# Performance work log

Hardware: AMD Instinct MI355X
Metric: run time of the kernel (lower is better)

Reference implementation:

```python
import jax, jax.numpy as jnp
import numpy as np

B, DIM, RANK, H, W = 16, 64, 32, 128, 128
E, K, BINS, FREQ_DIM, KS = 4, 2, 8, 64, 7
NOISE_STD = 1.0 / E


def dwconv(x, w, b, pad):
    # depthwise conv, NCHW, weight [C,1,kh,kw]
    y = jax.lax.conv_general_dilated(x, w, (1, 1), [(pad, pad), (pad, pad)],
        dimension_numbers=('NCHW', 'OIHW', 'NCHW'), feature_group_count=x.shape[1])
    return y + b[None, :, None, None]


def avgpool3(x):
    # AvgPool2d(3, stride=1, padding=1), count_include_pad=True -> sum/9
    s = jax.lax.reduce_window(x, 0.0, jax.lax.add, (1, 1, 3, 3), (1, 1, 1, 1),
        [(0, 0), (0, 0), (1, 1), (1, 1)])
    return s / 9.0


def freq_filter(x, gain, decay, cmax):
    # HighFreqGlobal / LowFreqGlobal: rfft2 -> scale magnitude by radial filter -> irfft2
    Bh, C, Hh, Wh = x.shape
    xf = jnp.fft.rfft2(x, norm='ortho')
    mag, ph = jnp.abs(xf), jnp.angle(xf)
    fy = jnp.fft.fftfreq(Hh).astype(x.dtype)[:, None]
    fx = jnp.fft.rfftfreq(Wh).astype(x.dtype)[None, :]
    fg = jnp.sqrt(fy ** 2 + fx ** 2)
    filt = jnp.clip((1.0 - jnp.exp(-gain * fg)) * jnp.exp(-decay * fg), 0.0, cmax)
    return jnp.fft.irfft2((mag * filt) * jnp.exp(1j * ph), s=(Hh, Wh), norm='ortho')


def freq_energy(x):
    # RoutingFunction.get_frequency_energy: radial energy histogram over BINS bins
    Bh, C, Hh, Wh = x.shape
    mag = jnp.abs(jnp.fft.fft2(x, norm='forward'))
    gy = jnp.arange(-Hh // 2, Hh // 2, dtype=jnp.float32)[:, None]
    gx = jnp.arange(-Wh // 2, Wh // 2, dtype=jnp.float32)[None, :]
    dist = jnp.sqrt(gy ** 2 + gx ** 2)
    edges = jnp.linspace(0.0, dist.max(), BINS + 1)
    masks = ((dist[None] >= edges[:-1, None, None]) & (dist[None] < edges[1:, None, None])).astype(mag.dtype)
    return jnp.einsum('bchw,khw->bk', mag, masks) / C  # sum over HW then mean over C


def setup_inputs():
    key = jax.random.key(0)
    ks = jax.random.split(key, 16)
    p = lambda k, shp, s=0.02: jax.random.normal(k, shp, jnp.float32) * s
    return {
        'x': jax.random.normal(ks[0], (B, DIM, H, W), jnp.float32),
        'noise': jax.random.normal(ks[1], (B, E), jnp.float32),
        'gate_w': p(ks[2], (E, DIM)),
        'fg_w1': p(ks[3], (FREQ_DIM, BINS)),
        'fg_b1': jnp.zeros((FREQ_DIM,), jnp.float32),
        'fg_w2': p(ks[4], (E, FREQ_DIM)),
        'proj0': p(ks[5], (E, RANK, DIM)),
        'proj1': p(ks[6], (E, RANK, DIM)),
        'proj2': p(ks[7], (E, DIM, RANK)),
        'hg_gain': jnp.float32(2.0),
        'hg_decay': jnp.float32(0.5),
        'hf_w1': p(ks[8], (RANK, 1, 3, 3), 0.1),
        'hf_b1': jnp.zeros((RANK,), jnp.float32),
        'hf_w2': p(ks[9], (RANK, 1, 3, 3), 0.1),
        'hf_b2': jnp.zeros((RANK,), jnp.float32),
        'lg_gain': jnp.float32(1.0),
        'lg_decay': jnp.float32(1.0),
        'lf_w': p(ks[10], (RANK, 1, KS, KS), 0.1),
        'lf_b': jnp.zeros((RANK,), jnp.float32),
    }


def reference(x, noise, gate_w, fg_w1, fg_b1, fg_w2, proj0, proj1, proj2,
              hg_gain, hg_decay, hf_w1, hf_b1, hf_w2, hf_b2,
              lg_gain, lg_decay, lf_w, lf_b):
    Bh = x.shape[0]
    # routing: image gate (GAP + linear) + frequency gate (MLP on radial energy)
    img_logits = jnp.mean(x, axis=(2, 3)) @ gate_w.T
    femb = freq_energy(x)
    hidden = jax.nn.relu(femb @ fg_w1.T + fg_b1)
    logits = img_logits + hidden @ fg_w2.T
    scores = jax.nn.softmax(logits + noise * NOISE_STD, axis=-1)
    vals, idx = jax.lax.top_k(scores, K)
    gates = jnp.zeros_like(scores).at[jnp.arange(Bh)[:, None], idx].set(vals)

    def expert(e, body):
        # ModExpert.process: low-rank proj -> body * silu(gate proj of shared=x) -> up proj + shortcut
        h = jnp.einsum('bchw,rc->brhw', x, proj0[e])
        g = jax.nn.silu(jnp.einsum('bchw,rc->brhw', x, proj1[e]))
        h = body(h) * g
        return jnp.einsum('brhw,cr->bchw', h, proj2[e]) + x

    gelu = lambda z: jax.nn.gelu(z, approximate=False)
    bodies = [
        lambda z: freq_filter(z, hg_gain, hg_decay, 3.0),                          # HighFreqGlobal
        lambda z: dwconv(gelu(dwconv(z, hf_w1, hf_b1, 1)), hf_w2, hf_b2, 1),       # HighFreqLocal
        lambda z: freq_filter(z, lg_gain, lg_decay, 1.0),                          # LowFreqGlobal
        lambda z: avgpool3(gelu(dwconv(z, lf_w, lf_b, KS // 2))),                  # LowFreqLocal
    ]
    # dispatch/combine expressed densely: gates are exactly zero for non-selected experts,
    # so weighted sum == SparseDispatcher.combine
    out = jnp.zeros_like(x)
    for e, body in enumerate(bodies):
        out = out + gates[:, e][:, None, None, None] * expert(e, body)
    return out
```

## Files before the change

### kernel.cpp

```cpp
#include <hip/hip_runtime.h>
#include <math.h>


namespace {

struct cpx { float x, y; };
struct TwB {
  cpx t0;
  cpx ws[6];
  float sg[6];
};

using bf16x8 = __attribute__((ext_vector_type(8))) short;
using f32x4  = __attribute__((ext_vector_type(4))) float;

__device__ __forceinline__ short f2bf(float f){
  unsigned u = __float_as_uint(f);
  u += 0x7FFF + ((u >> 16) & 1);
  return (short)(u >> 16);
}

__device__ __forceinline__ cpx cmul(cpx a, cpx b){ return {a.x*b.x - a.y*b.y, a.x*b.y + a.y*b.x}; }

__device__ __forceinline__ cpx tw(int k, float invN){
  float s, c;
  sincosf(-6.283185307179586f * (float)k * invN, &s, &c);
  return {c, s};
}

__device__ __forceinline__ void init_twb(TwB &T, int lane){
  T.t0 = tw(lane, 1.0f/128.0f);
  int m = 32;
  #pragma unroll
  for (int s = 0; s < 6; s++){
    bool up = (lane & m) != 0;
    cpx w = tw(lane & (m-1), 1.0f/(float)(2*m));
    T.ws[s] = up ? w : cpx{1.0f, 0.0f};
    T.sg[s] = up ? -1.0f : 1.0f;
    m >>= 1;
  }
}

__device__ __forceinline__ int br6(int l){ return (int)(__brev((unsigned)l) >> 26); }
__device__ __forceinline__ int pos7(int j){ return ((j & 1) << 6) | (j >> 1); }

__device__ __forceinline__ void fft128(cpx &a, cpx &b, int lane, const TwB &T){
  cpx u{a.x + b.x, a.y + b.y};
  cpx v{a.x - b.x, a.y - b.y};
  v = cmul(v, T.t0);
  a = u; b = v;
  int m = 32;
  #pragma unroll
  for (int s = 0; s < 6; s++){
    float pax = __shfl_xor(a.x, m);
    float pay = __shfl_xor(a.y, m);
    float pbx = __shfl_xor(b.x, m);
    float pby = __shfl_xor(b.y, m);
    float sg = T.sg[s];
    cpx w = T.ws[s];
    cpx ta{fmaf(sg, a.x, pax), fmaf(sg, a.y, pay)};
    cpx tb{fmaf(sg, b.x, pbx), fmaf(sg, b.y, pby)};
    a = cmul(ta, w);
    b = cmul(tb, w);
    m >>= 1;
  }
}

__device__ __forceinline__ float gelu_exact(float v){
  return 0.5f * v * (1.0f + erff(v * 0.70710678118654752f));
}

__device__ __forceinline__ float silu(float v){
  return v / (1.0f + expf(-v));
}


__global__ __launch_bounds__(512) void k_fft2fwd(const float* __restrict__ x, float2* __restrict__ X,
                                                 float* __restrict__ part_w, float* __restrict__ xmean){
  __shared__ float2 z[8192];
  int bc = blockIdx.x; int t = threadIdx.x;
  int lane = t & 63, wv = t >> 6;
  TwB T; init_twb(T, lane);
  const float* img = x + (size_t)bc * 16384;
  int rb = br6(lane);

  #pragma unroll 4
  for (int k = 0; k < 8; k++){
    int p = wv*8 + k;
    int h0 = 2*p, h1 = 2*p + 1;
    cpx a{img[h0*128 + lane],      img[h1*128 + lane]};
    cpx b{img[h0*128 + lane + 64], img[h1*128 + lane + 64]};
    fft128(a, b, lane, T);
    int ia = (p << 7) | (rb ^ p);
    z[ia]      = make_float2(a.x, a.y);
    z[ia | 64] = make_float2(b.x, b.y);
  }
  __syncthreads();

  float rax[8], ray[8], rbx[8], rby[8];
  #pragma unroll
  for (int k = 0; k < 8; k++){
    int jj = wv*8 + k;
    int p  = lane >> 1, s = lane & 1;
    int p2 = 32 + p;
    cpx a, b;
    if (jj == 0){
      float2 z0  = z[(p << 7)  | (0  ^ p)];
      float2 z64 = z[(p << 7)  | (32 ^ p)];
      float2 w0  = z[(p2 << 7) | (0  ^ p2)];
      float2 w64 = z[(p2 << 7) | (32 ^ p2)];
      a = { s ? z0.y : z0.x, s ? z64.y : z64.x };
      b = { s ? w0.y : w0.x, s ? w64.y : w64.x };
    } else {
      int jm = 128 - jj;
      int pj = pos7(jj), pm = pos7(jm);
      float2 z1 = z[(p << 7) | (pj ^ p)],  z2 = z[(p << 7) | (pm ^ p)];
      if (s == 0) a = { 0.5f*(z1.x + z2.x), 0.5f*(z1.y - z2.y) };
      else        a = { 0.5f*(z1.y + z2.y), 0.5f*(z2.x - z1.x) };
      float2 w1 = z[(p2 << 7) | (pj ^ p2)], w2 = z[(p2 << 7) | (pm ^ p2)];
      if (s == 0) b = { 0.5f*(w1.x + w2.x), 0.5f*(w1.y - w2.y) };
      else        b = { 0.5f*(w1.y + w2.y), 0.5f*(w2.x - w1.x) };
    }
    fft128(a, b, lane, T);
    rax[k] = a.x; ray[k] = a.y; rbx[k] = b.x; rby[k] = b.y;
  }
  __syncthreads();
  #pragma unroll
  for (int k = 0; k < 8; k++){
    int jj = wv*8 + k;
    int ia = (jj << 7) | (rb ^ jj);
    z[ia]      = make_float2(rax[k], ray[k]);
    z[ia | 64] = make_float2(rbx[k], rby[k]);
  }
  __syncthreads();

  if (t == 0) xmean[bc] = z[0].x * (1.0f/16384.0f);

  float edges[9];
  float step = sqrtf(8192.0f) * 0.125f;
  #pragma unroll
  for (int k = 0; k <= 8; k++) edges[k] = step * (float)k;
  float acc[8] = {0,0,0,0,0,0,0,0};
  for (int idx = t; idx < 64*128; idx += 512){
    int j = idx >> 7, i = idx & 127;
    if (j == 0){
      float2 c0 = z[pos7(i)];
      int in_ = (128 - i) & 127;
      float2 d0v = z[pos7(in_)];
      float x0r = 0.5f*(c0.x + d0v.x), x0i = 0.5f*(c0.y - d0v.y);
      float x6r = 0.5f*(c0.y + d0v.y), x6i = 0.5f*(d0v.x - c0.x);
      float m0 = sqrtf(x0r*x0r + x0i*x0i) * (1.0f/16384.0f);
      float m6 = sqrtf(x6r*x6r + x6i*x6i) * (1.0f/16384.0f);
      float dyv = (float)(i - 64);
      float d0 = sqrtf(dyv*dyv + 4096.0f);
      float d6 = fabsf(dyv);
      #pragma unroll
      for (int k = 0; k < 8; k++){
        if (d0 >= edges[k] && d0 < edges[k+1]) acc[k] += m0;
        if (d6 >= edges[k] && d6 < edges[k+1]) acc[k] += m6;
      }
    } else {
      float2 zv = z[(j << 7) | (pos7(i) ^ j)];
      float mag = sqrtf(zv.x*zv.x + zv.y*zv.y) * (2.0f/16384.0f);
      float dy = (float)(i - 64), dx = (float)(j - 64);
      float d = sqrtf(dy*dy + dx*dx);
      #pragma unroll
      for (int k = 0; k < 8; k++)
        if (d >= edges[k] && d < edges[k+1]) acc[k] += mag;
    }
  }
  #pragma unroll
  for (int k = 0; k < 8; k++){
    float v = acc[k];
    for (int off = 32; off > 0; off >>= 1) v += __shfl_xor(v, off);
    if (lane == 0) part_w[(bc*8 + wv)*8 + k] = v;
  }

  float2* Xo = X + (size_t)bc * (65*128);
  for (int idx = t; idx < 65*128; idx += 512){
    int j = idx >> 7, i = idx & 127;
    float2 v;
    if (j == 0){
      float2 c0 = z[pos7(i)];
      int in_ = (128 - i) & 127;
      float2 d0v = z[pos7(in_)];
      v = make_float2(0.5f*(c0.x + d0v.x), 0.5f*(c0.y - d0v.y));
    } else if (j == 64){
      float2 c0 = z[pos7(i)];
      int in_ = (128 - i) & 127;
      float2 d0v = z[pos7(in_)];
      v = make_float2(0.5f*(c0.y + d0v.y), 0.5f*(d0v.x - c0.x));
    } else {
      v = z[(j << 7) | (pos7(i) ^ j)];
    }
    Xo[idx] = v;
  }
}

__global__ __launch_bounds__(128) void k_routing(const float* __restrict__ xmean, const float* __restrict__ part_w,
    const float* __restrict__ noise, const float* __restrict__ gate_w,
    const float* __restrict__ fg_w1, const float* __restrict__ fg_b1, const float* __restrict__ fg_w2,
    int* __restrict__ slot_e, int* __restrict__ slot_of, float* __restrict__ slot_g){
  __shared__ float femb[16][8];
  __shared__ float hid[16][64];
  __shared__ float lgt[16][4];
  int t = threadIdx.x;
  {
    int b = t >> 3, k = t & 7;
    float s = 0.f;
    for (int c = 0; c < 64; c++)
      for (int w = 0; w < 8; w++)
        s += part_w[((b*64 + c)*8 + w)*8 + k];
    femb[b][k] = s * (1.0f/64.0f);
  }
  __syncthreads();
  for (int idx = t; idx < 16*64; idx += 128){
    int b = idx >> 6, f = idx & 63;
    float s = fg_b1[f];
    for (int k = 0; k < 8; k++) s += femb[b][k] * fg_w1[f*8 + k];
    hid[b][f] = fmaxf(s, 0.f);
  }
  __syncthreads();
  if (t < 64){
    int b = t >> 2, e = t & 3;
    float s = 0.f;
    for (int c = 0; c < 64; c++) s += xmean[b*64 + c] * gate_w[e*64 + c];
    for (int f = 0; f < 64; f++) s += hid[b][f] * fg_w2[e*64 + f];
    lgt[b][e] = s + noise[b*4 + e] * 0.25f;
  }
  __syncthreads();
  if (t < 16){
    int b = t;
    float m = fmaxf(fmaxf(lgt[b][0], lgt[b][1]), fmaxf(lgt[b][2], lgt[b][3]));
    float p[4]; float sum = 0.f;
    for (int e = 0; e < 4; e++){ p[e] = expf(lgt[b][e] - m); sum += p[e]; }
    for (int e = 0; e < 4; e++) p[e] /= sum;
    int i1 = 0;
    for (int e = 1; e < 4; e++) if (p[e] > p[i1]) i1 = e;
    int i2 = -1;
    for (int e = 0; e < 4; e++){ if (e == i1) continue; if (i2 < 0 || p[e] > p[i2]) i2 = e; }
    slot_e[b*2 + 0] = i1;
    slot_e[b*2 + 1] = i2;
    slot_g[b*2 + 0] = p[i1];
    slot_g[b*2 + 1] = p[i2];
    for (int e = 0; e < 4; e++) slot_of[b*4 + e] = (e == i1) ? 0 : ((e == i2) ? 1 : -1);
  }
}

__global__ __launch_bounds__(256) void k_transW(const float* __restrict__ proj0, float* __restrict__ p0t){
  int t = threadIdx.x;
  for (int idx = t; idx < 2048; idx += 256){
    int r = idx >> 6, c = idx & 63;
    p0t[0*2048 + c*32 + r] = proj0[0*2048 + idx];
    p0t[1*2048 + c*32 + r] = proj0[2*2048 + idx];
  }
}

__global__ __launch_bounds__(256) void k_projfreq(const float2* __restrict__ X, const float* __restrict__ p0t,
    float2* __restrict__ Y, const int* __restrict__ slot_e,
    const float* __restrict__ hg_gain, const float* __restrict__ hg_decay,
    const float* __restrict__ lg_gain, const float* __restrict__ lg_decay){
  int b = blockIdx.z;
  int e0 = __builtin_amdgcn_readfirstlane(slot_e[b*2 + 0]);
  int e1 = __builtin_amdgcn_readfirstlane(slot_e[b*2 + 1]);
  bool f0 = (e0 == 0) || (e0 == 2);
  bool f1 = (e1 == 0) || (e1 == 2);
  if (!f0 && !f1) return;
  int j = blockIdx.y;
  int i0 = blockIdx.x * 64;
  int t = threadIdx.x;
  int lane = t & 63;
  int w = __builtin_amdgcn_readfirstlane(t >> 6);
  __shared__ float2 sx[64][64];
  for (int idx = t; idx < 4096; idx += 256){
    int c = idx >> 6, ii = idx & 63;
    sx[c][ii] = X[(((size_t)(b*64 + c))*65 + j)*128 + i0 + ii];
  }
  __syncthreads();
  int i = i0 + lane;
  const float* W0 = p0t + ((f0 ? (e0 >> 1) : (e1 >> 1)) * 2048) + w*8;
  const float* W1 = p0t + ((f1 ? (e1 >> 1) : (e0 >> 1)) * 2048) + w*8;
  float a0x[8] = {0,0,0,0,0,0,0,0}, a0y[8] = {0,0,0,0,0,0,0,0};
  float a1x[8] = {0,0,0,0,0,0,0,0}, a1y[8] = {0,0,0,0,0,0,0,0};
  for (int c = 0; c < 64; c++){
    float2 xv = sx[c][lane];
    const float* wc0 = W0 + c*32;
    const float* wc1 = W1 + c*32;
    #pragma unroll
    for (int k = 0; k < 8; k++){
      float w0v = wc0[k];
      a0x[k] += w0v * xv.x; a0y[k] += w0v * xv.y;
      float w1v = wc1[k];
      a1x[k] += w1v * xv.x; a1y[k] += w1v * xv.y;
    }
  }
  float fy = (float)(i < 64 ? i : i - 128) * (1.0f/128.0f);
  float fx = (float)j * (1.0f/128.0f);
  float fg = sqrtf(fy*fy + fx*fx);
  if (f0){
    float gain, decay, cmax;
    if (e0 == 0){ gain = *hg_gain; decay = *hg_decay; cmax = 3.0f; }
    else        { gain = *lg_gain; decay = *lg_decay; cmax = 1.0f; }
    float filt = (1.0f - expf(-gain*fg)) * expf(-decay*fg);
    filt = fminf(fmaxf(filt, 0.0f), cmax) * (1.0f/16384.0f);
    int bs = b*2 + 0;
    #pragma unroll
    for (int k = 0; k < 8; k++){
      int r = w*8 + k;
      Y[((size_t)(bs*32 + r))*8320 + j*128 + i] = make_float2(a0x[k]*filt, a0y[k]*filt);
    }
  }
  if (f1){
    float gain, decay, cmax;
    if (e1 == 0){ gain = *hg_gain; decay = *hg_decay; cmax = 3.0f; }
    else        { gain = *lg_gain; decay = *lg_decay; cmax = 1.0f; }
    float filt = (1.0f - expf(-gain*fg)) * expf(-decay*fg);
    filt = fminf(fmaxf(filt, 0.0f), cmax) * (1.0f/16384.0f);
    int bs = b*2 + 1;
    #pragma unroll
    for (int k = 0; k < 8; k++){
      int r = w*8 + k;
      Y[((size_t)(bs*32 + r))*8320 + j*128 + i] = make_float2(a1x[k]*filt, a1y[k]*filt);
    }
  }
}

__global__ __launch_bounds__(512) void k_ifft2(float2* __restrict__ Y, const int* __restrict__ slot_e){
  int blk = blockIdx.x;
  int bs = blk >> 5, r = blk & 31;
  int es = slot_e[bs];
  if (es == 1 || es == 3) return;
  __shared__ float2 z[8192];
  int t = threadIdx.x; int lane = t & 63, wv = t >> 6;
  TwB T; init_twb(T, lane);
  int rb = br6(lane);
  float2* Yb = Y + (size_t)(bs*32 + r) * 8320;

  for (int idx = t; idx < 8192; idx += 512){
    int j = idx >> 7, i = idx & 127;
    if (j == 0){
      float2 y0 = Yb[i];
      float2 y6 = Yb[8192 + i];
      z[pos7(i)] = make_float2(y0.x - y6.y, y0.y + y6.x);
    } else {
      z[(j << 7) | (pos7(i) ^ j)] = Yb[idx];
    }
  }
  __syncthreads();

  #pragma unroll
  for (int k = 0; k < 8; k++){
    int jj = wv*8 + k;
    float2 z0 = z[(jj << 7) | (pos7(lane) ^ jj)];
    float2 z1 = z[(jj << 7) | ((pos7(lane) + 32) ^ jj)];
    cpx a{z0.x, -z0.y}, b{z1.x, -z1.y};
    fft128(a, b, lane, T);
    int ia = (jj << 7) | (rb ^ jj);
    z[ia]      = make_float2(a.x, -a.y);
    z[ia | 64] = make_float2(b.x, -b.y);
  }
  __syncthreads();

  float* body = (float*)Yb;
  #pragma unroll 2
  for (int k = 0; k < 8; k++){
    int p = wv*8 + k;
    int h = 2*p, h1 = 2*p + 1;
    int ph = pos7(h), ph1 = pos7(h1);
    cpx a, b;
    if (lane == 0){
      float2 c0 = z[ph], c1 = z[ph1];
      a = { c0.x, c1.x };
      b = { c0.y, c1.y };
    } else {
      float2 yh = z[(lane << 7) | (ph ^ lane)];
      float2 y1 = z[(lane << 7) | (ph1 ^ lane)];
      a = { yh.x - y1.y, yh.y + y1.x };
      int lm = 64 - lane;
      float2 zh  = z[(lm << 7) | (ph ^ lm)];
      float2 z1_ = z[(lm << 7) | (ph1 ^ lm)];
      b = { zh.x + z1_.y, z1_.x - zh.y };
    }
    a.y = -a.y; b.y = -b.y;
    fft128(a, b, lane, T);
    int n0 = 2*rb;
    body[h*128 + n0]      = a.x;
    body[h1*128 + n0]     = -a.y;
    body[h*128 + n0 + 1]  = b.x;
    body[h1*128 + n0 + 1] = -b.y;
  }
}

__global__ __launch_bounds__(256) void k_projA(const float* __restrict__ x, const float* __restrict__ proj0,
    const int* __restrict__ slot_e, float* __restrict__ A){
  int b = blockIdx.y;
  int e0 = __builtin_amdgcn_readfirstlane(slot_e[b*2 + 0]);
  int e1 = __builtin_amdgcn_readfirstlane(slot_e[b*2 + 1]);
  bool c0 = (e0 == 1) || (e0 == 3);
  bool c1 = (e1 == 1) || (e1 == 3);
  if (!c0 && !c1) return;
  __shared__ unsigned short xs[128][72];
  int px0 = blockIdx.x * 128;
  int t = threadIdx.x;
  int w = t >> 6, lane = t & 63;
  int h = lane & 15, g = lane >> 4;
  const float* xb = x + (size_t)b*64*16384;

  for (int idx = t; idx < 2048; idx += 256){
    int c = idx >> 5, pq = idx & 31;
    float4 v = *(const float4*)&xb[(size_t)c*16384 + px0 + pq*4];
    xs[pq*4 + 0][c] = (unsigned short)f2bf(v.x);
    xs[pq*4 + 1][c] = (unsigned short)f2bf(v.y);
    xs[pq*4 + 2][c] = (unsigned short)f2bf(v.z);
    xs[pq*4 + 3][c] = (unsigned short)f2bf(v.w);
  }

  bf16x8 af[2][2][2];
  #pragma unroll
  for (int s = 0; s < 2; s++){
    bool cv = (s == 0) ? c0 : c1;
    if (!cv) continue;
    int e = (s == 0) ? e0 : e1;
    const float* P0 = proj0 + e*2048;
    #pragma unroll
    for (int mr = 0; mr < 2; mr++)
      #pragma unroll
      for (int k0 = 0; k0 < 2; k0++){
        const float* p = P0 + (mr*16 + h)*64 + k0*32 + g*8;
        bf16x8 v;
        #pragma unroll
        for (int j = 0; j < 8; j++) v[j] = f2bf(p[j]);
        af[s][mr][k0] = v;
      }
  }
  __syncthreads();

  int pxw = w*32;
  #pragma unroll
  for (int nt = 0; nt < 2; nt++){
    int pxl = pxw + nt*16;
    int px  = px0 + pxl;
    bf16x8 bx[2];
    #pragma unroll
    for (int k0 = 0; k0 < 2; k0++)
      bx[k0] = *(bf16x8*)&xs[pxl + h][k0*32 + g*8];
    #pragma unroll
    for (int s = 0; s < 2; s++){
      bool cv = (s == 0) ? c0 : c1;
      if (!cv) continue;
      float* Ab = A + (size_t)((b*2 + s)*32)*16384;
      #pragma unroll
      for (int mr = 0; mr < 2; mr++){
        f32x4 acc = {0.f, 0.f, 0.f, 0.f};
        acc = __builtin_amdgcn_mfma_f32_16x16x32_bf16(af[s][mr][0], bx[0], acc, 0, 0, 0);
        acc = __builtin_amdgcn_mfma_f32_16x16x32_bf16(af[s][mr][1], bx[1], acc, 0, 0, 0);
        #pragma unroll
        for (int reg = 0; reg < 4; reg++){
          int r = mr*16 + g*4 + reg;
          Ab[(size_t)r*16384 + px + h] = acc[reg];
        }
      }
    }
  }
}

__global__ __launch_bounds__(256) void k_conv3(const float* __restrict__ A, float* __restrict__ bodyY,
    const float* __restrict__ w1g, const float* __restrict__ b1g,
    const float* __restrict__ w2g, const float* __restrict__ b2g,
    const int* __restrict__ slot_of){
  int by = blockIdx.y; int b = by >> 5, r = by & 31;
  int slot = slot_of[b*4 + 1];
  if (slot < 0) return;
  int bs = b*2 + slot;
  int h0 = blockIdx.x * 16;
  int t = threadIdx.x;
  __shared__ float sin_[20*130];
  __shared__ float st[18*130];
  for (int i = t; i < 20*130; i += 256) sin_[i] = 0.f;
  for (int i = t; i < 18*130; i += 256) st[i] = 0.f;
  float w1[9], w2[9];
  #pragma unroll
  for (int k = 0; k < 9; k++){ w1[k] = w1g[r*9 + k]; w2[k] = w2g[r*9 + k]; }
  float b1 = b1g[r], b2 = b2g[r];
  __syncthreads();
  const float* ip = A + (size_t)(bs*32 + r)*16384;
  for (int idx = t; idx < 20*128; idx += 256){
    int li = idx >> 7, ww = idx & 127;
    int ih = h0 - 2 + li;
    if (ih >= 0 && ih < 128) sin_[li*130 + 1 + ww] = ip[ih*128 + ww];
  }
  __syncthreads();
  for (int idx = t; idx < 18*128; idx += 256){
    int li = idx >> 7, ww = idx & 127;
    int hs = h0 - 1 + li;
    if (hs >= 0 && hs < 128){
      float acc = b1;
      #pragma unroll
      for (int kh = 0; kh < 3; kh++)
        #pragma unroll
        for (int kw = 0; kw < 3; kw++)
          acc += w1[kh*3 + kw] * sin_[(li + kh)*130 + ww + kw];
      st[li*130 + 1 + ww] = gelu_exact(acc);
    }
  }
  __syncthreads();
  float* op = bodyY + (size_t)(bs*32 + r)*16640;
  for (int idx = t; idx < 16*128; idx += 256){
    int li = idx >> 7, ww = idx & 127;
    int ho = h0 + li;
    float acc = b2;
    #pragma unroll
    for (int kh = 0; kh < 3; kh++)
      #pragma unroll
      for (int kw = 0; kw < 3; kw++)
        acc += w2[kh*3 + kw] * st[(li + kh)*130 + ww + kw];
    op[ho*128 + ww] = acc;
  }
}

__global__ __launch_bounds__(256) void k_conv7(const float* __restrict__ A, float* __restrict__ bodyY,
    const float* __restrict__ wg, const float* __restrict__ bg,
    const int* __restrict__ slot_of){
  int by = blockIdx.y; int b = by >> 5, r = by & 31;
  int slot = slot_of[b*4 + 3];
  if (slot < 0) return;
  int bs = b*2 + slot;
  int h0 = blockIdx.x * 16;
  int t = threadIdx.x;
  __shared__ float sin_[24*134];
  __shared__ float st[18*134];
  __shared__ float wsh[49];
  for (int i = t; i < 24*134; i += 256) sin_[i] = 0.f;
  for (int i = t; i < 18*134; i += 256) st[i] = 0.f;
  if (t < 49) wsh[t] = wg[r*49 + t];
  float bias = bg[r];
  __syncthreads();
  const float* ip = A + (size_t)(bs*32 + r)*16384;
  for (int idx = t; idx < 24*128; idx += 256){
    int li = idx >> 7, ww = idx & 127;
    int ih = h0 - 4 + li;
    if (ih >= 0 && ih < 128) sin_[li*134 + 3 + ww] = ip[ih*128 + ww];
  }
  __syncthreads();
  for (int idx = t; idx < 18*128; idx += 256){
    int li = idx >> 7, ww = idx & 127;
    int hs = h0 - 1 + li;
    if (hs >= 0 && hs < 128){
      float acc = bias;
      #pragma unroll
      for (int kh = 0; kh < 7; kh++)
        #pragma unroll
        for (int kw = 0; kw < 7; kw++)
          acc += wsh[kh*7 + kw] * sin_[(li + kh)*134 + ww + kw];
      st[li*134 + 1 + ww] = gelu_exact(acc);
    }
  }
  __syncthreads();
  float* op = bodyY + (size_t)(bs*32 + r)*16640;
  for (int idx = t; idx < 16*128; idx += 256){
    int li = idx >> 7, ww = idx & 127;
    int ho = h0 + li;
    float acc = 0.f;
    #pragma unroll
    for (int kh = 0; kh < 3; kh++)
      #pragma unroll
      for (int kw = 0; kw < 3; kw++)
        acc += st[(li + kh)*134 + ww + kw];
    op[ho*128 + ww] = acc * (1.0f/9.0f);
  }
}

__global__ __launch_bounds__(256) void k_combine(const float* __restrict__ x, const float* __restrict__ bodyY,
    const float* __restrict__ proj1, const float* __restrict__ proj2,
    const int* __restrict__ slot_e, const float* __restrict__ slot_g,
    float* __restrict__ out){
  __shared__ unsigned short xs[128][72];
  __shared__ unsigned short bs2[2][128][36];
  __shared__ unsigned short sblk[4][2][16][40];
  int b = blockIdx.y;
  int px0 = blockIdx.x * 128;
  int t = threadIdx.x;
  int w = t >> 6, lane = t & 63;
  int h = lane & 15, g = lane >> 4;
  int ea = __builtin_amdgcn_readfirstlane(slot_e[b*2 + 0]);
  int eb = __builtin_amdgcn_readfirstlane(slot_e[b*2 + 1]);
  float ga = slot_g[b*2 + 0], gb = slot_g[b*2 + 1];
  float gs = ga + gb;

  const float* xb = x + (size_t)b*64*16384;
  float* ob = out + (size_t)b*64*16384;
  const float* Bd0 = bodyY + (size_t)(b*2 + 0)*32*16640;
  const float* Bd1 = bodyY + (size_t)(b*2 + 1)*32*16640;

  for (int idx = t; idx < 2048; idx += 256){
    int c = idx >> 5, pq = idx & 31;
    float4 v = *(const float4*)&xb[(size_t)c*16384 + px0 + pq*4];
    xs[pq*4 + 0][c] = (unsigned short)f2bf(v.x);
    xs[pq*4 + 1][c] = (unsigned short)f2bf(v.y);
    xs[pq*4 + 2][c] = (unsigned short)f2bf(v.z);
    xs[pq*4 + 3][c] = (unsigned short)f2bf(v.w);
  }
  for (int idx = t; idx < 2048; idx += 256){
    int s = idx >> 10, r = (idx >> 5) & 31, pq = idx & 31;
    const float* Bod = (s == 0) ? Bd0 : Bd1;
    float4 v = *(const float4*)&Bod[(size_t)r*16640 + px0 + pq*4];
    bs2[s][pq*4 + 0][r] = (unsigned short)f2bf(v.x);
    bs2[s][pq*4 + 1][r] = (unsigned short)f2bf(v.y);
    bs2[s][pq*4 + 2][r] = (unsigned short)f2bf(v.z);
    bs2[s][pq*4 + 3][r] = (unsigned short)f2bf(v.w);
  }

  bf16x8 a1[2][2][2];
  #pragma unroll
  for (int s = 0; s < 2; s++){
    const float* P1 = proj1 + (s == 0 ? ea : eb)*2048;
    #pragma unroll
    for (int mr = 0; mr < 2; mr++)
      #pragma unroll
      for (int k0 = 0; k0 < 2; k0++){
        const float* p = P1 + (mr*16 + h)*64 + k0*32 + g*8;
        bf16x8 v;
        #pragma unroll
        for (int j = 0; j < 8; j++) v[j] = f2bf(p[j]);
        a1[s][mr][k0] = v;
      }
  }
  bf16x8 a2[2][4];
  #pragma unroll
  for (int s = 0; s < 2; s++){
    const float* P2 = proj2 + (s == 0 ? ea : eb)*2048;
    #pragma unroll
    for (int mc = 0; mc < 4; mc++){
      const float* p = P2 + (mc*16 + h)*32 + g*8;
      bf16x8 v;
      #pragma unroll
      for (int j = 0; j < 8; j++) v[j] = f2bf(p[j]);
      a2[s][mc] = v;
    }
  }
  __syncthreads();

  int pxw = w*32;
  #pragma unroll
  for (int nt = 0; nt < 2; nt++){
    int pxl = pxw + nt*16;
    int px  = px0 + pxl;
    bf16x8 bx[2];
    #pragma unroll
    for (int k0 = 0; k0 < 2; k0++)
      bx[k0] = *(bf16x8*)&xs[pxl + h][k0*32 + g*8];
    f32x4 acc1[2][2];
    #pragma unroll
    for (int s = 0; s < 2; s++)
      #pragma unroll
      for (int mr = 0; mr < 2; mr++){
        f32x4 acc = {0.f, 0.f, 0.f, 0.f};
        acc = __builtin_amdgcn_mfma_f32_16x16x32_bf16(a1[s][mr][0], bx[0], acc, 0, 0, 0);
        acc = __builtin_amdgcn_mfma_f32_16x16x32_bf16(a1[s][mr][1], bx[1], acc, 0, 0, 0);
        acc1[s][mr] = acc;
      }
    #pragma unroll
    for (int s = 0; s < 2; s++){
      float gw = (s == 0) ? ga : gb;
      #pragma unroll
      for (int mr = 0; mr < 2; mr++){
        int r0 = mr*16 + g*4;
        unsigned short b4[4];
        *(uint2*)b4 = *(uint2*)&bs2[s][pxl + h][r0];
        unsigned pk0, pk1;
        {
          float bv0 = __uint_as_float(((unsigned)b4[0]) << 16);
          float bv1 = __uint_as_float(((unsigned)b4[1]) << 16);
          float bv2 = __uint_as_float(((unsigned)b4[2]) << 16);
          float bv3 = __uint_as_float(((unsigned)b4[3]) << 16);
          float s0 = gw * bv0 * silu(acc1[s][mr][0]);
          float s1 = gw * bv1 * silu(acc1[s][mr][1]);
          float s2 = gw * bv2 * silu(acc1[s][mr][2]);
          float s3 = gw * bv3 * silu(acc1[s][mr][3]);
          pk0 = (unsigned)(unsigned short)f2bf(s0) | ((unsigned)(unsigned short)f2bf(s1) << 16);
          pk1 = (unsigned)(unsigned short)f2bf(s2) | ((unsigned)(unsigned short)f2bf(s3) << 16);
        }
        uint2 pv; pv.x = pk0; pv.y = pk1;
        *(uint2*)&sblk[w][s][h][r0] = pv;
      }
    }
    bf16x8 sb0 = *(bf16x8*)&sblk[w][0][h][g*8];
    bf16x8 sb1 = *(bf16x8*)&sblk[w][1][h][g*8];
    f32x4 acc2[4];
    #pragma unroll
    for (int mc = 0; mc < 4; mc++){
      f32x4 acc = {0.f, 0.f, 0.f, 0.f};
      acc = __builtin_amdgcn_mfma_f32_16x16x32_bf16(a2[0][mc], sb0, acc, 0, 0, 0);
      acc = __builtin_amdgcn_mfma_f32_16x16x32_bf16(a2[1][mc], sb1, acc, 0, 0, 0);
      acc2[mc] = acc;
    }
    #pragma unroll
    for (int mc = 0; mc < 4; mc++)
      #pragma unroll
      for (int reg = 0; reg < 4; reg++){
        int c = mc*16 + g*4 + reg;
        size_t o = (size_t)c*16384 + px + h;
        ob[o] = gs * xb[o] + acc2[mc][reg];
      }
  }
}

}

extern "C" void kernel_launch(void* const* d_in, const int* in_sizes, int n_in,
                              void* d_out, int out_size, void* d_ws, size_t ws_size,
                              hipStream_t stream) {
  (void)in_sizes; (void)n_in; (void)out_size; (void)ws_size;
  const float* x        = (const float*)d_in[0];
  const float* noise    = (const float*)d_in[1];
  const float* gate_w   = (const float*)d_in[2];
  const float* fg_w1    = (const float*)d_in[3];
  const float* fg_b1    = (const float*)d_in[4];
  const float* fg_w2    = (const float*)d_in[5];
  const float* proj0    = (const float*)d_in[6];
  const float* proj1    = (const float*)d_in[7];
  const float* proj2    = (const float*)d_in[8];
  const float* hg_gain  = (const float*)d_in[9];
  const float* hg_decay = (const float*)d_in[10];
  const float* hf_w1    = (const float*)d_in[11];
  const float* hf_b1    = (const float*)d_in[12];
  const float* hf_w2    = (const float*)d_in[13];
  const float* hf_b2    = (const float*)d_in[14];
  const float* lg_gain  = (const float*)d_in[15];
  const float* lg_decay = (const float*)d_in[16];
  const float* lf_w     = (const float*)d_in[17];
  const float* lf_b     = (const float*)d_in[18];
  float* out = (float*)d_out;

  float* ws = (float*)d_ws;
  float2* X  = (float2*)ws;
  float*  A  = ws;
  float*  Yf = ws + 17039360;
  float2* Y2 = (float2*)Yf;
  float*  tail   = ws + 34078720;
  float*  xmean  = tail;
  float*  part_w = xmean + 1024;
  float*  p0t    = part_w + 65536;
  float*  slot_g = p0t + 4096;
  int*    slot_e = (int*)(slot_g + 32);
  int*    slot_of = slot_e + 32;

  k_transW<<<1, 256, 0, stream>>>(proj0, p0t);
  k_fft2fwd<<<1024, 512, 0, stream>>>(x, X, part_w, xmean);
  k_routing<<<1, 128, 0, stream>>>(xmean, part_w, noise, gate_w, fg_w1, fg_b1, fg_w2,
                                   slot_e, slot_of, slot_g);

  k_projfreq<<<dim3(2,65,16), 256, 0, stream>>>(X, p0t, Y2, slot_e,
                                                hg_gain, hg_decay, lg_gain, lg_decay);

  k_projA<<<dim3(128,16), 256, 0, stream>>>(x, proj0, slot_e, A);

  k_ifft2<<<1024, 512, 0, stream>>>(Y2, slot_e);

  k_conv3<<<dim3(8,512), 256, 0, stream>>>(A, Yf, hf_w1, hf_b1, hf_w2, hf_b2, slot_of);
  k_conv7<<<dim3(8,512), 256, 0, stream>>>(A, Yf, lf_w, lf_b, slot_of);

  k_combine<<<dim3(128,16), 256, 0, stream>>>(x, Yf, proj1, proj2, slot_e, slot_g, out);
}
```

Before: 304.6 us.

## Precompute FFT twiddles into a table and stage combine output for float4 stores

Twiddle factors are now computed once by the transpose kernel into a 128-entry global table, and the FFT kernels read from that table instead of calling sincosf per lane per stage. The combine kernel now stages its MFMA results in a shared-memory buffer that aliases the earlier tiles, then writes the output with coalesced float4 loads and stores that fuse in the shortcut term. This replaces the old scattered per-element global writes. It adds a __syncthreads and a larger shared footprint, which may lower occupancy.

```diff
diff --git a/kernel.cpp b/kernel.cpp
--- a/kernel.cpp
+++ b/kernel.cpp
@@ -22,20 +22,15 @@
 
 __device__ __forceinline__ cpx cmul(cpx a, cpx b){ return {a.x*b.x - a.y*b.y, a.x*b.y + a.y*b.x}; }
 
-__device__ __forceinline__ cpx tw(int k, float invN){
-  float s, c;
-  sincosf(-6.283185307179586f * (float)k * invN, &s, &c);
-  return {c, s};
-}
-
-__device__ __forceinline__ void init_twb(TwB &T, int lane){
-  T.t0 = tw(lane, 1.0f/128.0f);
+__device__ __forceinline__ void init_twb(TwB &T, int lane, const float2* __restrict__ tw128){
+  float2 v0 = tw128[lane];
+  T.t0 = {v0.x, v0.y};
   int m = 32;
   #pragma unroll
   for (int s = 0; s < 6; s++){
     bool up = (lane & m) != 0;
-    cpx w = tw(lane & (m-1), 1.0f/(float)(2*m));
-    T.ws[s] = up ? w : cpx{1.0f, 0.0f};
+    float2 wv = tw128[(lane & (m-1)) * (64/m)];
+    T.ws[s] = up ? cpx{wv.x, wv.y} : cpx{1.0f, 0.0f};
     T.sg[s] = up ? -1.0f : 1.0f;
     m >>= 1;
   }
@@ -75,12 +70,28 @@
 }
 
 
+__global__ __launch_bounds__(256) void k_transW(const float* __restrict__ proj0, float* __restrict__ p0t,
+                                                float2* __restrict__ tw128){
+  int t = threadIdx.x;
+  if (t < 128){
+    float s, c;
+    sincosf(-6.283185307179586f * (float)t * (1.0f/128.0f), &s, &c);
+    tw128[t] = make_float2(c, s);
+  }
+  for (int idx = t; idx < 2048; idx += 256){
+    int r = idx >> 6, c = idx & 63;
+    p0t[0*2048 + c*32 + r] = proj0[0*2048 + idx];
+    p0t[1*2048 + c*32 + r] = proj0[2*2048 + idx];
+  }
+}
+
 __global__ __launch_bounds__(512) void k_fft2fwd(const float* __restrict__ x, float2* __restrict__ X,
-                                                 float* __restrict__ part_w, float* __restrict__ xmean){
+                                                 float* __restrict__ part_w, float* __restrict__ xmean,
+                                                 const float2* __restrict__ tw128){
   __shared__ float2 z[8192];
   int bc = blockIdx.x; int t = threadIdx.x;
   int lane = t & 63, wv = t >> 6;
-  TwB T; init_twb(T, lane);
+  TwB T; init_twb(T, lane, tw128);
   const float* img = x + (size_t)bc * 16384;
   int rb = br6(lane);
 
@@ -247,15 +258,6 @@
   }
 }
 
-__global__ __launch_bounds__(256) void k_transW(const float* __restrict__ proj0, float* __restrict__ p0t){
-  int t = threadIdx.x;
-  for (int idx = t; idx < 2048; idx += 256){
-    int r = idx >> 6, c = idx & 63;
-    p0t[0*2048 + c*32 + r] = proj0[0*2048 + idx];
-    p0t[1*2048 + c*32 + r] = proj0[2*2048 + idx];
-  }
-}
-
 __global__ __launch_bounds__(256) void k_projfreq(const float2* __restrict__ X, const float* __restrict__ p0t,
     float2* __restrict__ Y, const int* __restrict__ slot_e,
     const float* __restrict__ hg_gain, const float* __restrict__ hg_decay,
@@ -325,14 +327,15 @@
   }
 }
 
-__global__ __launch_bounds__(512) void k_ifft2(float2* __restrict__ Y, const int* __restrict__ slot_e){
+__global__ __launch_bounds__(512) void k_ifft2(float2* __restrict__ Y, const int* __restrict__ slot_e,
+                                               const float2* __restrict__ tw128){
   int blk = blockIdx.x;
   int bs = blk >> 5, r = blk & 31;
   int es = slot_e[bs];
   if (es == 1 || es == 3) return;
   __shared__ float2 z[8192];
   int t = threadIdx.x; int lane = t & 63, wv = t >> 6;
-  TwB T; init_twb(T, lane);
+  TwB T; init_twb(T, lane, tw128);
   int rb = br6(lane);
   float2* Yb = Y + (size_t)(bs*32 + r) * 8320;
 
@@ -574,9 +577,12 @@
     const float* __restrict__ proj1, const float* __restrict__ proj2,
     const int* __restrict__ slot_e, const float* __restrict__ slot_g,
     float* __restrict__ out){
-  __shared__ unsigned short xs[128][72];
-  __shared__ unsigned short bs2[2][128][36];
-  __shared__ unsigned short sblk[4][2][16][40];
+  __shared__ __align__(16) unsigned char smem[57344];
+  unsigned short (*xs)[72]            = (unsigned short(*)[72])(smem);
+  unsigned short (*bs2)[128][36]      = (unsigned short(*)[128][36])(smem + 18432);
+  unsigned short (*sblk)[4][2][16][40] = (unsigned short(*)[4][2][16][40])(smem + 36864);
+  float* obuf = (float*)smem;
+
   int b = blockIdx.y;
   int px0 = blockIdx.x * 128;
   int t = threadIdx.x;
@@ -644,7 +650,6 @@
   #pragma unroll
   for (int nt = 0; nt < 2; nt++){
     int pxl = pxw + nt*16;
-    int px  = px0 + pxl;
     bf16x8 bx[2];
     #pragma unroll
     for (int k0 = 0; k0 < 2; k0++)
@@ -681,27 +686,38 @@
           pk1 = (unsigned)(unsigned short)f2bf(s2) | ((unsigned)(unsigned short)f2bf(s3) << 16);
         }
         uint2 pv; pv.x = pk0; pv.y = pk1;
-        *(uint2*)&sblk[w][s][h][r0] = pv;
+        *(uint2*)&sblk[nt][w][s][h][r0] = pv;
       }
     }
-    bf16x8 sb0 = *(bf16x8*)&sblk[w][0][h][g*8];
-    bf16x8 sb1 = *(bf16x8*)&sblk[w][1][h][g*8];
-    f32x4 acc2[4];
+  }
+  __syncthreads();
+
+  #pragma unroll
+  for (int nt = 0; nt < 2; nt++){
+    bf16x8 sb0 = *(bf16x8*)&sblk[nt][w][0][h][g*8];
+    bf16x8 sb1 = *(bf16x8*)&sblk[nt][w][1][h][g*8];
     #pragma unroll
     for (int mc = 0; mc < 4; mc++){
       f32x4 acc = {0.f, 0.f, 0.f, 0.f};
       acc = __builtin_amdgcn_mfma_f32_16x16x32_bf16(a2[0][mc], sb0, acc, 0, 0, 0);
       acc = __builtin_amdgcn_mfma_f32_16x16x32_bf16(a2[1][mc], sb1, acc, 0, 0, 0);
-      acc2[mc] = acc;
-    }
-    #pragma unroll
-    for (int mc = 0; mc < 4; mc++)
       #pragma unroll
       for (int reg = 0; reg < 4; reg++){
         int c = mc*16 + g*4 + reg;
-        size_t o = (size_t)c*16384 + px + h;
-        ob[o] = gs * xb[o] + acc2[mc][reg];
+        obuf[(w*64 + c)*36 + nt*16 + h] = acc[reg];
       }
+    }
+  }
+  int fq = lane & 7, cr = lane >> 3;
+  const float* xw = xb + px0 + w*32;
+  float* ow = ob + px0 + w*32;
+  #pragma unroll
+  for (int i = 0; i < 8; i++){
+    int c = i*8 + cr;
+    float4 v = *(float4*)&obuf[(w*64 + c)*36 + fq*4];
+    float4 xv4 = *(const float4*)&xw[(size_t)c*16384 + fq*4];
+    *(float4*)&ow[(size_t)c*16384 + fq*4] =
+      make_float4(gs*xv4.x + v.x, gs*xv4.y + v.y, gs*xv4.z + v.z, gs*xv4.w + v.w);
   }
 }
 
@@ -741,12 +757,14 @@
   float*  xmean  = tail;
   float*  part_w = xmean + 1024;
   float*  p0t    = part_w + 65536;
-  float*  slot_g = p0t + 4096;
+  float*  tw128f = p0t + 4096;
+  float2* tw128  = (float2*)tw128f;
+  float*  slot_g = tw128f + 256;
   int*    slot_e = (int*)(slot_g + 32);
   int*    slot_of = slot_e + 32;
 
-  k_transW<<<1, 256, 0, stream>>>(proj0, p0t);
-  k_fft2fwd<<<1024, 512, 0, stream>>>(x, X, part_w, xmean);
+  k_transW<<<1, 256, 0, stream>>>(proj0, p0t, tw128);
+  k_fft2fwd<<<1024, 512, 0, stream>>>(x, X, part_w, xmean, tw128);
   k_routing<<<1, 128, 0, stream>>>(xmean, part_w, noise, gate_w, fg_w1, fg_b1, fg_w2,
                                    slot_e, slot_of, slot_g);
 
@@ -755,7 +773,7 @@
 
   k_projA<<<dim3(128,16), 256, 0, stream>>>(x, proj0, slot_e, A);
 
-  k_ifft2<<<1024, 512, 0, stream>>>(Y2, slot_e);
+  k_ifft2<<<1024, 512, 0, stream>>>(Y2, slot_e, tw128);
 
   k_conv3<<<dim3(8,512), 256, 0, stream>>>(A, Yf, hf_w1, hf_b1, hf_w2, hf_b2, slot_of);
   k_conv7<<<dim3(8,512), 256, 0, stream>>>(A, Yf, lf_w, lf_b, slot_of);
```

New measurement: 306.3 us. No clear change (+0.5%).
